# Performance work log

Hardware: AMD Instinct MI355X
Metric: run time of the kernel (lower is better)

The kernel has to match this reference:

```python
import jax, jax.numpy as jnp
import numpy as np

IN_DIM = 128
NUM_IDX = 128
LATENT = 512
FF_HID = 4 * IN_DIM
EPS = 1e-5


def _layernorm(x, g, b):
    mu = jnp.mean(x, axis=-1, keepdims=True)
    var = jnp.mean((x - mu) ** 2, axis=-1, keepdims=True)
    return (x - mu) * jax.lax.rsqrt(var + EPS) * g + b


def setup_inputs() -> dict:
    key = jax.random.key(0)
    ks = jax.random.split(key, 12)
    B, N, D, L = 16, NUM_IDX, IN_DIM, LATENT
    s = lambda fan_in: 1.0 / np.sqrt(fan_in)
    return {
        "in_obs": jax.random.normal(ks[0], (B, N, D), jnp.float32),
        "Wq_w": jax.random.normal(ks[1], (D, L), jnp.float32) * s(D),
        "Wq_b": jax.random.normal(ks[2], (L,), jnp.float32) * s(D),
        "Wk_w": jax.random.normal(ks[3], (D, L), jnp.float32) * s(D),
        "Wk_b": jax.random.normal(ks[4], (L,), jnp.float32) * s(D),
        "wv_w": jax.random.normal(ks[5], (2 * L + 2 * N,), jnp.float32) * s(2 * L + 2 * N),
        "wv_b": jax.random.normal(ks[6], (), jnp.float32) * s(2 * L + 2 * N),
        "g1": jnp.ones((D,), jnp.float32),
        "b1": jnp.zeros((D,), jnp.float32),
        "ff1_w": jax.random.normal(ks[7], (D, FF_HID), jnp.float32) * s(D),
        "ff1_b": jax.random.normal(ks[8], (FF_HID,), jnp.float32) * s(D),
        "ff2_w": jax.random.normal(ks[9], (FF_HID, D), jnp.float32) * s(FF_HID),
        "ff2_b": jax.random.normal(ks[10], (D,), jnp.float32) * s(FF_HID),
        "g2": jnp.ones((D,), jnp.float32),
        "b2": jnp.zeros((D,), jnp.float32),
    }


def reference(in_obs, Wq_w, Wq_b, Wk_w, Wk_b, wv_w, wv_b, g1, b1,
              ff1_w, ff1_b, ff2_w, ff2_b, g2, b2):
    # in_obs: [B, N, D]
    B, N, D = in_obs.shape
    L = Wq_w.shape[1]
    eye = jnp.broadcast_to(jnp.eye(N, dtype=in_obs.dtype), (B, N, N))
    # q_cat/k_cat: [B, N, L+N]
    q_cat = jnp.concatenate([in_obs @ Wq_w + Wq_b, eye], axis=-1)
    k_cat = jnp.concatenate([in_obs @ Wk_w + Wk_b, eye], axis=-1)
    # Original: w_v(tanh(concat(q_i, k_j))). tanh is elementwise and the dot
    # product splits over the concat, so score[b,i,j] = a[b,i] + c[b,j] + bias
    # -- mathematically identical, avoids the [B,N,N,2L+2N] intermediate.
    a = jnp.tanh(q_cat) @ wv_w[: L + N]          # [B, N]
    c = jnp.tanh(k_cat) @ wv_w[L + N:]           # [B, N]
    scores = a[:, :, None] + c[:, None, :] + wv_b  # [B, N, N]
    weights = jax.nn.softmax(scores, axis=-1)
    attn = weights @ in_obs                       # [B, N, D]
    res = _layernorm(attn + in_obs, g1, b1)
    ff = jax.nn.relu(res @ ff1_w + ff1_b) @ ff2_w + ff2_b
    return _layernorm(ff + in_obs, g2, b2)
```

## Files before the change

### kernel.cpp

```cpp
#include <hip/hip_runtime.h>

#define NN 128
#define DD 128
#define LL 512
#define FFH 512
#define TANH1 0.76159415595576489f

typedef __attribute__((ext_vector_type(8))) short bf16x8;
typedef __attribute__((ext_vector_type(4))) float f32x4;

struct alignas(16) f4arr { float v[4]; };

__device__ __forceinline__ unsigned short f2bf(float f) {
    union { float f; unsigned u; } v; v.f = f;
    return (unsigned short)((v.u + 0x7FFFu + ((v.u >> 16) & 1u)) >> 16);
}

__global__ __launch_bounds__(256) void kScores(
    const float* __restrict__ in_obs,
    const float* __restrict__ Wk_w,
    const float* __restrict__ Wk_b,
    const float* __restrict__ wv_w,
    float* __restrict__ c_out)
{
    const int t = threadIdx.x;
    const int wave = t >> 6, lane = t & 63;
    __shared__ float row_lds[8][128];
    __shared__ float red[8][4];

    const int row0 = blockIdx.x * 8;
    const float* src = in_obs + row0 * DD;
    #pragma unroll
    for (int i = 0; i < 4; ++i) {
        int idx = t + i * 256;
        row_lds[idx >> 7][idx & 127] = src[idx];
    }
    __syncthreads();

    const int l0 = t, l1 = t + 256;
    float acc0[8], acc1[8];
    #pragma unroll
    for (int r = 0; r < 8; ++r) { acc0[r] = 0.f; acc1[r] = 0.f; }

    #pragma unroll 4
    for (int d = 0; d < 128; d += 4) {
        f4arr rbuf[8];
        #pragma unroll
        for (int r = 0; r < 8; ++r)
            rbuf[r] = *(const f4arr*)&row_lds[r][d];
        #pragma unroll
        for (int dd = 0; dd < 4; ++dd) {
            const float w0 = Wk_w[(d + dd) * LL + l0];
            const float w1 = Wk_w[(d + dd) * LL + l1];
            #pragma unroll
            for (int r = 0; r < 8; ++r) {
                acc0[r] += rbuf[r].v[dd] * w0;
                acc1[r] += rbuf[r].v[dd] * w1;
            }
        }
    }
    const float kb0 = Wk_b[l0], kb1 = Wk_b[l1];
    const float wv0 = wv_w[640 + l0], wv1 = wv_w[640 + l1];
    float v[8];
    #pragma unroll
    for (int r = 0; r < 8; ++r)
        v[r] = tanhf(acc0[r] + kb0) * wv0 + tanhf(acc1[r] + kb1) * wv1;
    #pragma unroll
    for (int off = 32; off > 0; off >>= 1) {
        #pragma unroll
        for (int r = 0; r < 8; ++r)
            v[r] += __shfl_down(v[r], off, 64);
    }
    if (lane == 0) {
        #pragma unroll
        for (int r = 0; r < 8; ++r) red[r][wave] = v[r];
    }
    __syncthreads();
    if (t < 8) {
        const int row = row0 + t;
        const int j = row & (NN - 1);
        c_out[row] = red[t][0] + red[t][1] + red[t][2] + red[t][3]
                   + TANH1 * wv_w[1152 + j];
    }
}

__global__ __launch_bounds__(256) void kPrep(
    const float* __restrict__ ff1_w,
    const float* __restrict__ ff2_w,
    unsigned short* __restrict__ W1f,
    unsigned short* __restrict__ W2f)
{
    const int t = threadIdx.x;
    const int bi = blockIdx.x;
    const int fg = bi & 127;
    const int jp = t >> 6;
    const int lane = t & 63;
    const int l15 = lane & 15, l4 = lane >> 4;
    const int j = jp * 2;
    unsigned short v0, v1;
    unsigned short* dst;
    if (bi < 128) {
        const int ks = fg & 3, mt = fg >> 2;
        v0 = f2bf(ff1_w[(ks * 32 + l4 * 8 + j    ) * FFH + mt * 16 + l15]);
        v1 = f2bf(ff1_w[(ks * 32 + l4 * 8 + j + 1) * FFH + mt * 16 + l15]);
        dst = W1f;
    } else {
        const int ks = fg & 15, mt = fg >> 4;
        v0 = f2bf(ff2_w[(ks * 32 + l4 * 8 + j    ) * DD + mt * 16 + l15]);
        v1 = f2bf(ff2_w[(ks * 32 + l4 * 8 + j + 1) * DD + mt * 16 + l15]);
        dst = W2f;
    }
    *(unsigned*)&dst[(fg * 64 + lane) * 8 + j] = (unsigned)v0 | ((unsigned)v1 << 16);
}

__global__ __launch_bounds__(512, 2) void kB(
    const float* __restrict__ in_obs,
    const float* __restrict__ c_in,
    const unsigned short* __restrict__ W1f,
    const unsigned short* __restrict__ W2f,
    const float* __restrict__ g1, const float* __restrict__ b1,
    const float* __restrict__ ff1_b,
    const float* __restrict__ ff2_b,
    const float* __restrict__ g2, const float* __restrict__ b2,
    float* __restrict__ out)
{
    const int t = threadIdx.x;
    const int b = blockIdx.x >> 4;
    const int j0 = (blockIdx.x & 15) * 8;
    const int wave = t >> 6, lane = t & 63;
    const int l15 = lane & 15, l4 = lane >> 4;

    __shared__ float part[8][128];
    __shared__ alignas(16) unsigned short res_lds[16 * 128];
    __shared__ alignas(16) unsigned short h_lds[16 * 512];
    __shared__ alignas(16) float o2_lds[16 * 128];

    bf16x8 a1p[16];
    #pragma unroll
    for (int i = 0; i < 4; ++i)
        #pragma unroll
        for (int ks = 0; ks < 4; ++ks)
            a1p[i * 4 + ks] =
                *(const bf16x8*)(W1f + (((wave * 4 + i) * 4 + ks) * 64 + lane) * 8);
    bf16x8 a2p[16];
    #pragma unroll
    for (int ks = 0; ks < 16; ++ks)
        a2p[ks] = *(const bf16x8*)(W2f + ((wave * 16 + ks) * 64 + lane) * 8);

    const float cv0 = c_in[b * NN + lane];
    const float cv1 = c_in[b * NN + lane + 64];
    float mx = fmaxf(cv0, cv1);
    #pragma unroll
    for (int off = 32; off > 0; off >>= 1) mx = fmaxf(mx, __shfl_xor(mx, off, 64));
    float e0 = __expf(cv0 - mx), e1 = __expf(cv1 - mx);
    float sm = e0 + e1;
    #pragma unroll
    for (int off = 32; off > 0; off >>= 1) sm += __shfl_xor(sm, off, 64);
    const float inv = 1.f / sm;
    e0 *= inv; e1 *= inv;

    {
        const float* base = in_obs + (b * NN + wave * 16) * DD;
        float a0 = 0.f, a1 = 0.f;
        #pragma unroll
        for (int jj = 0; jj < 16; ++jj) {
            const int js = wave * 16 + jj;
            const float wj = (wave < 4) ? __shfl(e0, js, 64)
                                        : __shfl(e1, js - 64, 64);
            a0 += wj * base[jj * DD + lane];
            a1 += wj * base[jj * DD + 64 + lane];
        }
        part[wave][lane] = a0;
        part[wave][lane + 64] = a1;
    }
    __syncthreads();

    {
        const int r = wave;
        const int row = b * NN + j0 + r;
        const int c0i = lane * 2;
        const float2 xo = *(const float2*)&in_obs[row * DD + c0i];
        float x0 = xo.x, x1 = xo.y;
        #pragma unroll
        for (int g = 0; g < 8; ++g) {
            const float2 p = *(const float2*)&part[g][c0i];
            x0 += p.x; x1 += p.y;
        }
        float s = x0 + x1;
        #pragma unroll
        for (int off = 32; off > 0; off >>= 1) s += __shfl_xor(s, off, 64);
        const float mu = s * (1.f / 128.f);
        const float d0 = x0 - mu, d1 = x1 - mu;
        float vs = d0 * d0 + d1 * d1;
        #pragma unroll
        for (int off = 32; off > 0; off >>= 1) vs += __shfl_xor(vs, off, 64);
        const float rstd = rsqrtf(vs * (1.f / 128.f) + 1e-5f);
        const float2 gv = *(const float2*)&g1[c0i];
        const float2 bv = *(const float2*)&b1[c0i];
        const float r0 = d0 * rstd * gv.x + bv.x;
        const float r1 = d1 * rstd * gv.y + bv.y;
        const unsigned pk = (unsigned)f2bf(r0) | ((unsigned)f2bf(r1) << 16);
        const int swz = (lane * 4) ^ ((r & 7) << 4);
        *(unsigned*)((char*)res_lds + r * 256 + swz) = pk;
        *(unsigned*)((char*)res_lds + (r + 8) * 256 + (lane * 4)) = 0u;
    }
    __syncthreads();

    {
        bf16x8 bfrag[4];
        #pragma unroll
        for (int ks = 0; ks < 4; ++ks) {
            const int off = l15 * 256 + ((ks * 64 + l4 * 16) ^ ((l15 & 7) << 4));
            bfrag[ks] = *(const bf16x8*)((const char*)res_lds + off);
        }
        #pragma unroll
        for (int i = 0; i < 4; ++i) {
            const int mt = wave * 4 + i;
            f32x4 acc = {0.f, 0.f, 0.f, 0.f};
            #pragma unroll
            for (int ks = 0; ks < 4; ++ks)
                acc = __builtin_amdgcn_mfma_f32_16x16x32_bf16(
                          a1p[i * 4 + ks], bfrag[ks], acc, 0, 0, 0);
            const f4arr bias = *(const f4arr*)&ff1_b[mt * 16 + l4 * 4];
            uint2 pk;
            pk.x = (unsigned)f2bf(fmaxf(acc[0] + bias.v[0], 0.f))
                 | ((unsigned)f2bf(fmaxf(acc[1] + bias.v[1], 0.f)) << 16);
            pk.y = (unsigned)f2bf(fmaxf(acc[2] + bias.v[2], 0.f))
                 | ((unsigned)f2bf(fmaxf(acc[3] + bias.v[3], 0.f)) << 16);
            const int off = l15 * 1024 + ((mt * 32 + l4 * 8) ^ ((l15 & 7) << 4));
            *(uint2*)((char*)h_lds + off) = pk;
        }
    }
    __syncthreads();

    {
        f32x4 acc = {0.f, 0.f, 0.f, 0.f};
        #pragma unroll
        for (int ks = 0; ks < 16; ++ks) {
            const int off = l15 * 1024 + ((ks * 64 + l4 * 16) ^ ((l15 & 7) << 4));
            const bf16x8 bfrag = *(const bf16x8*)((const char*)h_lds + off);
            acc = __builtin_amdgcn_mfma_f32_16x16x32_bf16(a2p[ks], bfrag, acc, 0, 0, 0);
        }
        const int off = l15 * 512 + ((wave * 64 + l4 * 16) ^ ((l15 & 7) << 4));
        *(f32x4*)((char*)o2_lds + off) = acc;
    }
    __syncthreads();

    {
        const int r = wave;
        const int row = b * NN + j0 + r;
        const int c0i = lane * 2;
        const int off = r * 512 + ((lane * 8) ^ ((r & 7) << 4));
        const float2 o2 = *(const float2*)((char*)o2_lds + off);
        const float2 fb = *(const float2*)&ff2_b[c0i];
        const float2 xo = *(const float2*)&in_obs[row * DD + c0i];
        const float f0 = o2.x + fb.x + xo.x;
        const float f1 = o2.y + fb.y + xo.y;
        float s = f0 + f1;
        #pragma unroll
        for (int off2 = 32; off2 > 0; off2 >>= 1) s += __shfl_xor(s, off2, 64);
        const float mu = s * (1.f / 128.f);
        const float d0 = f0 - mu, d1 = f1 - mu;
        float vs = d0 * d0 + d1 * d1;
        #pragma unroll
        for (int off2 = 32; off2 > 0; off2 >>= 1) vs += __shfl_xor(vs, off2, 64);
        const float rstd = rsqrtf(vs * (1.f / 128.f) + 1e-5f);
        const float2 gv = *(const float2*)&g2[c0i];
        const float2 bv = *(const float2*)&b2[c0i];
        float2 o;
        o.x = d0 * rstd * gv.x + bv.x;
        o.y = d1 * rstd * gv.y + bv.y;
        *(float2*)&out[row * DD + c0i] = o;
    }
}

extern "C" void kernel_launch(void* const* d_in, const int* in_sizes, int n_in,
                              void* d_out, int out_size, void* d_ws, size_t ws_size,
                              hipStream_t stream) {
    const float* in_obs = (const float*)d_in[0];
    const float* Wk_w  = (const float*)d_in[3];
    const float* Wk_b  = (const float*)d_in[4];
    const float* wv_w  = (const float*)d_in[5];
    const float* g1    = (const float*)d_in[7];
    const float* b1    = (const float*)d_in[8];
    const float* ff1_w = (const float*)d_in[9];
    const float* ff1_b = (const float*)d_in[10];
    const float* ff2_w = (const float*)d_in[11];
    const float* ff2_b = (const float*)d_in[12];
    const float* g2    = (const float*)d_in[13];
    const float* b2    = (const float*)d_in[14];
    float* outp = (float*)d_out;

    unsigned short* W1f = (unsigned short*)d_ws;
    unsigned short* W2f = W1f + 65536;
    float* c_ws = (float*)((char*)d_ws + 262144);

    kScores<<<256, 256, 0, stream>>>(in_obs, Wk_w, Wk_b, wv_w, c_ws);
    kPrep<<<256, 256, 0, stream>>>(ff1_w, ff2_w, W1f, W2f);
    kB<<<256, 512, 0, stream>>>(in_obs, c_ws, W1f, W2f, g1, b1,
                                ff1_b, ff2_b, g2, b2, outp);
}
```

Baseline: 26.36 us.

## Merge three kernels into one cooperative kernel with a grid sync

Fuses the score kernel, the weight-prep kernel and the main attention/FFN kernel into a single cooperative launch. A grid-wide barrier separates the score and bf16 weight-packing phase from the consumer phase. The score phase now uses 512 threads per block, one latent column each. This removes two kernel launches and the gaps between them, at the cost of a grid-sync barrier and a cooperative launch whose 256 blocks must all be co-resident.

```diff
diff --git a/kernel.cpp b/kernel.cpp
--- a/kernel.cpp
+++ b/kernel.cpp
@@ -1,4 +1,7 @@
 #include <hip/hip_runtime.h>
+#include <hip/hip_cooperative_groups.h>
+
+namespace cg = cooperative_groups;
 
 #define NN 128
 #define DD 128
@@ -16,125 +19,109 @@
     return (unsigned short)((v.u + 0x7FFFu + ((v.u >> 16) & 1u)) >> 16);
 }
 
-__global__ __launch_bounds__(256) void kScores(
+__global__ __launch_bounds__(512, 2) void k_coop(
     const float* __restrict__ in_obs,
     const float* __restrict__ Wk_w,
     const float* __restrict__ Wk_b,
     const float* __restrict__ wv_w,
-    float* __restrict__ c_out)
-{
-    const int t = threadIdx.x;
-    const int wave = t >> 6, lane = t & 63;
-    __shared__ float row_lds[8][128];
-    __shared__ float red[8][4];
-
-    const int row0 = blockIdx.x * 8;
-    const float* src = in_obs + row0 * DD;
-    #pragma unroll
-    for (int i = 0; i < 4; ++i) {
-        int idx = t + i * 256;
-        row_lds[idx >> 7][idx & 127] = src[idx];
-    }
-    __syncthreads();
-
-    const int l0 = t, l1 = t + 256;
-    float acc0[8], acc1[8];
-    #pragma unroll
-    for (int r = 0; r < 8; ++r) { acc0[r] = 0.f; acc1[r] = 0.f; }
-
-    #pragma unroll 4
-    for (int d = 0; d < 128; d += 4) {
-        f4arr rbuf[8];
-        #pragma unroll
-        for (int r = 0; r < 8; ++r)
-            rbuf[r] = *(const f4arr*)&row_lds[r][d];
-        #pragma unroll
-        for (int dd = 0; dd < 4; ++dd) {
-            const float w0 = Wk_w[(d + dd) * LL + l0];
-            const float w1 = Wk_w[(d + dd) * LL + l1];
-            #pragma unroll
-            for (int r = 0; r < 8; ++r) {
-                acc0[r] += rbuf[r].v[dd] * w0;
-                acc1[r] += rbuf[r].v[dd] * w1;
-            }
-        }
-    }
-    const float kb0 = Wk_b[l0], kb1 = Wk_b[l1];
-    const float wv0 = wv_w[640 + l0], wv1 = wv_w[640 + l1];
-    float v[8];
-    #pragma unroll
-    for (int r = 0; r < 8; ++r)
-        v[r] = tanhf(acc0[r] + kb0) * wv0 + tanhf(acc1[r] + kb1) * wv1;
-    #pragma unroll
-    for (int off = 32; off > 0; off >>= 1) {
-        #pragma unroll
-        for (int r = 0; r < 8; ++r)
-            v[r] += __shfl_down(v[r], off, 64);
-    }
-    if (lane == 0) {
-        #pragma unroll
-        for (int r = 0; r < 8; ++r) red[r][wave] = v[r];
-    }
-    __syncthreads();
-    if (t < 8) {
-        const int row = row0 + t;
-        const int j = row & (NN - 1);
-        c_out[row] = red[t][0] + red[t][1] + red[t][2] + red[t][3]
-                   + TANH1 * wv_w[1152 + j];
-    }
-}
-
-__global__ __launch_bounds__(256) void kPrep(
     const float* __restrict__ ff1_w,
     const float* __restrict__ ff2_w,
-    unsigned short* __restrict__ W1f,
-    unsigned short* __restrict__ W2f)
-{
-    const int t = threadIdx.x;
-    const int bi = blockIdx.x;
-    const int fg = bi & 127;
-    const int jp = t >> 6;
-    const int lane = t & 63;
-    const int l15 = lane & 15, l4 = lane >> 4;
-    const int j = jp * 2;
-    unsigned short v0, v1;
-    unsigned short* dst;
-    if (bi < 128) {
-        const int ks = fg & 3, mt = fg >> 2;
-        v0 = f2bf(ff1_w[(ks * 32 + l4 * 8 + j    ) * FFH + mt * 16 + l15]);
-        v1 = f2bf(ff1_w[(ks * 32 + l4 * 8 + j + 1) * FFH + mt * 16 + l15]);
-        dst = W1f;
-    } else {
-        const int ks = fg & 15, mt = fg >> 4;
-        v0 = f2bf(ff2_w[(ks * 32 + l4 * 8 + j    ) * DD + mt * 16 + l15]);
-        v1 = f2bf(ff2_w[(ks * 32 + l4 * 8 + j + 1) * DD + mt * 16 + l15]);
-        dst = W2f;
-    }
-    *(unsigned*)&dst[(fg * 64 + lane) * 8 + j] = (unsigned)v0 | ((unsigned)v1 << 16);
-}
-
-__global__ __launch_bounds__(512, 2) void kB(
-    const float* __restrict__ in_obs,
-    const float* __restrict__ c_in,
-    const unsigned short* __restrict__ W1f,
-    const unsigned short* __restrict__ W2f,
     const float* __restrict__ g1, const float* __restrict__ b1,
     const float* __restrict__ ff1_b,
     const float* __restrict__ ff2_b,
     const float* __restrict__ g2, const float* __restrict__ b2,
+    unsigned short* __restrict__ W1f,
+    unsigned short* __restrict__ W2f,
+    float* __restrict__ c_ws,
     float* __restrict__ out)
 {
     const int t = threadIdx.x;
-    const int b = blockIdx.x >> 4;
-    const int j0 = (blockIdx.x & 15) * 8;
+    const int blk = blockIdx.x;
     const int wave = t >> 6, lane = t & 63;
     const int l15 = lane & 15, l4 = lane >> 4;
 
+    __shared__ float row_lds[8][128];
+    __shared__ float red[8][8];
     __shared__ float part[8][128];
     __shared__ alignas(16) unsigned short res_lds[16 * 128];
     __shared__ alignas(16) unsigned short h_lds[16 * 512];
     __shared__ alignas(16) float o2_lds[16 * 128];
 
+    {
+        const int fl = t >> 3;
+        const int j  = t & 7;
+        const int fl15 = fl & 15, fl4 = fl >> 4;
+        if (blk < 128) {
+            const int ks = blk & 3, mt = blk >> 2;
+            W1f[(blk * 64 + fl) * 8 + j] =
+                f2bf(ff1_w[(ks * 32 + fl4 * 8 + j) * FFH + mt * 16 + fl15]);
+        } else {
+            const int fg = blk - 128;
+            const int ks = fg & 15, mt = fg >> 4;
+            W2f[(fg * 64 + fl) * 8 + j] =
+                f2bf(ff2_w[(ks * 32 + fl4 * 8 + j) * DD + mt * 16 + fl15]);
+        }
+    }
+
+    {
+        const int row0 = blk * 8;
+        const float* src = in_obs + row0 * DD;
+        #pragma unroll
+        for (int i = 0; i < 2; ++i) {
+            const int idx = t + i * 512;
+            row_lds[idx >> 7][idx & 127] = src[idx];
+        }
+        __syncthreads();
+
+        const int l = t;
+        float acc[8];
+        #pragma unroll
+        for (int r = 0; r < 8; ++r) acc[r] = 0.f;
+        #pragma unroll 4
+        for (int d = 0; d < 128; d += 4) {
+            f4arr rb[8];
+            #pragma unroll
+            for (int r = 0; r < 8; ++r)
+                rb[r] = *(const f4arr*)&row_lds[r][d];
+            #pragma unroll
+            for (int dd = 0; dd < 4; ++dd) {
+                const float w = Wk_w[(d + dd) * LL + l];
+                #pragma unroll
+                for (int r = 0; r < 8; ++r)
+                    acc[r] += rb[r].v[dd] * w;
+            }
+        }
+        const float kb = Wk_b[l];
+        const float wv = wv_w[640 + l];
+        float v[8];
+        #pragma unroll
+        for (int r = 0; r < 8; ++r)
+            v[r] = tanhf(acc[r] + kb) * wv;
+        #pragma unroll
+        for (int off = 32; off > 0; off >>= 1) {
+            #pragma unroll
+            for (int r = 0; r < 8; ++r)
+                v[r] += __shfl_down(v[r], off, 64);
+        }
+        if (lane == 0) {
+            #pragma unroll
+            for (int r = 0; r < 8; ++r) red[r][wave] = v[r];
+        }
+        __syncthreads();
+        if (t < 8) {
+            float s = TANH1 * wv_w[1152 + ((row0 + t) & (NN - 1))];
+            #pragma unroll
+            for (int g = 0; g < 8; ++g) s += red[t][g];
+            c_ws[row0 + t] = s;
+        }
+    }
+
+    __threadfence();
+    cg::this_grid().sync();
+
+    const int b = blk >> 4;
+    const int j0 = (blk & 15) * 8;
+
     bf16x8 a1p[16];
     #pragma unroll
     for (int i = 0; i < 4; ++i)
@@ -147,8 +134,8 @@
     for (int ks = 0; ks < 16; ++ks)
         a2p[ks] = *(const bf16x8*)(W2f + ((wave * 16 + ks) * 64 + lane) * 8);
 
-    const float cv0 = c_in[b * NN + lane];
-    const float cv1 = c_in[b * NN + lane + 64];
+    const float cv0 = c_ws[b * NN + lane];
+    const float cv1 = c_ws[b * NN + lane + 64];
     float mx = fmaxf(cv0, cv1);
     #pragma unroll
     for (int off = 32; off > 0; off >>= 1) mx = fmaxf(mx, __shfl_xor(mx, off, 64));
@@ -295,8 +282,12 @@
     unsigned short* W2f = W1f + 65536;
     float* c_ws = (float*)((char*)d_ws + 262144);
 
-    kScores<<<256, 256, 0, stream>>>(in_obs, Wk_w, Wk_b, wv_w, c_ws);
-    kPrep<<<256, 256, 0, stream>>>(ff1_w, ff2_w, W1f, W2f);
-    kB<<<256, 512, 0, stream>>>(in_obs, c_ws, W1f, W2f, g1, b1,
-                                ff1_b, ff2_b, g2, b2, outp);
+    void* args[] = {
+        (void*)&in_obs, (void*)&Wk_w, (void*)&Wk_b, (void*)&wv_w,
+        (void*)&ff1_w, (void*)&ff2_w, (void*)&g1, (void*)&b1,
+        (void*)&ff1_b, (void*)&ff2_b, (void*)&g2, (void*)&b2,
+        (void*)&W1f, (void*)&W2f, (void*)&c_ws, (void*)&outp
+    };
+    hipLaunchCooperativeKernel((const void*)k_coop, dim3(256), dim3(512),
+                               args, 0, stream);
 }
```

After: 78.50 us. 198% more time.
